# Kernel tuning notes

Measured on AMD Instinct MI355X. Metric: run time of the kernel, lower is better.

The kernel has to match this reference:

```python
import jax, jax.numpy as jnp
import numpy as np

D_MODEL = 1024
NUM_HEADS = 16
HEAD_DIM = D_MODEL // NUM_HEADS
R = 1.0
LAM = 0.1
CLIP_MIN = -15.0
CLIP_MAX = 15.0
EPS = 1e-9


def setup_inputs() -> dict:
    key = jax.random.key(0)
    k1, k2 = jax.random.split(key, 2)
    B, S = 2, 2048
    x = jax.random.normal(k1, (B, S, D_MODEL), dtype=jnp.float32)
    # NonNeg-constrained dense kernel -> nonnegative uniform init (small scale)
    W = jax.random.uniform(k2, (D_MODEL, D_MODEL), dtype=jnp.float32) * 0.02
    b = jnp.zeros((D_MODEL,), dtype=jnp.float32)
    d_q = jnp.ones((D_MODEL,), dtype=jnp.float32)
    d_k = jnp.ones((D_MODEL,), dtype=jnp.float32)
    d_v = jnp.ones((D_MODEL,), dtype=jnp.float32)
    return {"x": x, "W": W, "b": b, "d_q": d_q, "d_k": d_k, "d_v": d_v}


def _convex_r_softmax(z):
    z = jnp.clip(z, CLIP_MIN, CLIP_MAX)
    numerator = jax.nn.relu(jnp.exp(z - R) + LAM * z)
    denominator = jnp.sum(numerator, axis=-1, keepdims=True) + EPS
    return numerator / denominator


def reference(x, W, b, d_q, d_k, d_v):
    B, S, _ = x.shape
    x_proj = x @ W + b                      # [B, S, D]
    # diagonal scaling then split heads: [B, H, S, Dh]
    def heads(t):
        return t.reshape(B, S, NUM_HEADS, HEAD_DIM).transpose(0, 2, 1, 3)
    Q = heads(x_proj * d_q)
    K = heads(x_proj * d_k)
    V = heads(x_proj * d_v)
    scores = jnp.einsum('bhqd,bhkd->bhqk', Q, K)   # [B, H, S, S]
    attn = _convex_r_softmax(scores)
    out = jnp.einsum('bhqk,bhkd->bhqd', attn, V)   # [B, H, S, Dh]
    return out.transpose(0, 2, 1, 3).reshape(B, S, D_MODEL)
```

## Files before the change

kernel.cpp:

```cpp
#include <hip/hip_runtime.h>
#include <math.h>

#define D_MODEL   1024
#define NUM_HEADS 16
#define HEAD_DIM  64
#define S_LEN     2048
#define BATCH     2
#define M_TOT     (BATCH * S_LEN)

typedef __attribute__((ext_vector_type(8))) short short8;
typedef __attribute__((ext_vector_type(4))) short short4v;
typedef __attribute__((ext_vector_type(4))) float f32x4;

static __device__ __forceinline__ short f2bf(float f) {
    unsigned u = __builtin_bit_cast(unsigned, f);
    unsigned r = (u + 0x7FFFu + ((u >> 16) & 1u)) >> 16;
    return (short)r;
}

typedef __attribute__((address_space(3))) void lds_v;
typedef const __attribute__((address_space(1))) void glb_v;
static __device__ __forceinline__ void gll16(const void* g, void* l) {
    __builtin_amdgcn_global_load_lds((glb_v*)g, (lds_v*)l, 16, 0, 0);
}


__global__ __launch_bounds__(256) void cvt_x_kernel(
    const float* __restrict__ x, short* __restrict__ xb)
{
    int i = (blockIdx.x * 256 + threadIdx.x) * 8;
    float4 a = *(const float4*)(x + i);
    float4 b = *(const float4*)(x + i + 4);
    short8 o;
    o[0] = f2bf(a.x); o[1] = f2bf(a.y); o[2] = f2bf(a.z); o[3] = f2bf(a.w);
    o[4] = f2bf(b.x); o[5] = f2bf(b.y); o[6] = f2bf(b.z); o[7] = f2bf(b.w);
    *(short8*)(xb + i) = o;
}

__global__ __launch_bounds__(256) void cvt_w_kernel(
    const float* __restrict__ W, short* __restrict__ wt)
{
    __shared__ short T[64][72];
    const int tid = threadIdx.x;
    const int k0 = blockIdx.y * 64, n0 = blockIdx.x * 64;
    const int r = tid >> 4, c4 = (tid & 15) * 4;
    #pragma unroll
    for (int i = 0; i < 4; i++) {
        int kr = r + 16 * i;
        float4 v = *(const float4*)(W + (size_t)(k0 + kr) * D_MODEL + n0 + c4);
        short4v s;
        s[0] = f2bf(v.x); s[1] = f2bf(v.y); s[2] = f2bf(v.z); s[3] = f2bf(v.w);
        *(short4v*)&T[kr][c4] = s;
    }
    __syncthreads();
    const int n = tid >> 2, kb = (tid & 3) * 16;
    short tmp[16];
    #pragma unroll
    for (int j = 0; j < 16; j++) tmp[j] = T[kb + j][n];
    *(short8*)(wt + (size_t)(n0 + n) * D_MODEL + k0 + kb)     = *(short8*)&tmp[0];
    *(short8*)(wt + (size_t)(n0 + n) * D_MODEL + k0 + kb + 8) = *(short8*)&tmp[8];
}

__global__ __launch_bounds__(256) void gemm_qkv_kernel(
    const short* __restrict__ xb, const short* __restrict__ wt,
    const float* __restrict__ bias, const float* __restrict__ dq,
    const float* __restrict__ dk, const float* __restrict__ dv,
    short* __restrict__ Q, short* __restrict__ K, short* __restrict__ Vt)
{
    __shared__ __attribute__((aligned(16))) short lds[17408];

    const int tid  = threadIdx.x;
    const int w    = tid >> 6, l = tid & 63;
    const int quad = l >> 4,  c = l & 15;
    const int cx   = c & 7;
    const int n0 = blockIdx.x * 128, m0 = blockIdx.y * 128;
    const int wm = (w & 1) * 64, wn = (w >> 1) * 64;
    short* As = lds;
    short* Bs = lds + 8192;

    const int srow  = l >> 3;
    const int sslot = (l & 7) ^ srow;

    f32x4 acc[4][4];
    #pragma unroll
    for (int mi = 0; mi < 4; mi++)
        #pragma unroll
        for (int ni = 0; ni < 4; ni++) acc[mi][ni] = (f32x4){0.f, 0.f, 0.f, 0.f};

    for (int k0 = 0; k0 < D_MODEL; k0 += 64) {
        __syncthreads();
        #pragma unroll
        for (int i = 0; i < 4; i++) {
            int rbase = w * 32 + i * 8;
            int row = rbase + srow;
            gll16(xb + (size_t)(m0 + row) * D_MODEL + k0 + sslot * 8, As + rbase * 64);
            gll16(wt + (size_t)(n0 + row) * D_MODEL + k0 + sslot * 8, Bs + rbase * 64);
        }
        __syncthreads();
        #pragma unroll
        for (int kh = 0; kh < 2; kh++) {
            const int sx = (kh * 4 + quad) ^ cx;
            short8 af[4], bf[4];
            #pragma unroll
            for (int mi = 0; mi < 4; mi++)
                af[mi] = *(const short8*)&As[(wm + 16 * mi + c) * 64 + sx * 8];
            #pragma unroll
            for (int ni = 0; ni < 4; ni++)
                bf[ni] = *(const short8*)&Bs[(wn + 16 * ni + c) * 64 + sx * 8];
            #pragma unroll
            for (int mi = 0; mi < 4; mi++)
                #pragma unroll
                for (int ni = 0; ni < 4; ni++)
                    acc[mi][ni] = __builtin_amdgcn_mfma_f32_16x16x32_bf16(
                        af[mi], bf[ni], acc[mi][ni], 0, 0, 0);
        }
    }

    __syncthreads();
    const int b      = m0 >> 11;
    const int s_base = m0 & 2047;
    const int h      = (n0 + wn) >> 6;

    float biasv[4], dqv[4], dkv[4], dvv[4];
    #pragma unroll
    for (int ni = 0; ni < 4; ni++) {
        int n_g = n0 + wn + 16 * ni + c;
        biasv[ni] = bias[n_g]; dqv[ni] = dq[n_g];
        dkv[ni] = dk[n_g];     dvv[ni] = dv[n_g];
    }

    short* E = lds;
    #pragma unroll
    for (int mi = 0; mi < 4; mi++) {
        #pragma unroll
        for (int ni = 0; ni < 4; ni++) {
            short4v vv;
            #pragma unroll
            for (int r = 0; r < 4; r++) {
                float xv = acc[mi][ni][r] + biasv[ni];
                int s = s_base + wm + 16 * mi + 4 * quad + r;
                size_t off = (((size_t)(b * NUM_HEADS + h) * S_LEN + s) << 6) + (16 * ni + c);
                Q[off] = f2bf(xv * dqv[ni]);
                K[off] = f2bf(xv * dkv[ni]);
                vv[r]  = f2bf(xv * dvv[ni]);
            }
            int n_l = wn + 16 * ni + c;
            int m_l = wm + 16 * mi + 4 * quad;
            *(short4v*)&E[n_l * 136 + m_l] = vv;
        }
    }
    __syncthreads();
    {
        const int n_l = tid >> 1, mh = (tid & 1) * 64;
        const int h2 = (n0 + n_l) >> 6;
        const int dh = n_l & 63;
        short* dst = Vt + ((size_t)(b * NUM_HEADS + h2) * HEAD_DIM + dh) * S_LEN + s_base;
        #pragma unroll
        for (int ch = 0; ch < 8; ch++) {
            short8 v = *(const short8*)&E[n_l * 136 + mh + ch * 8];
            *(short8*)(dst + mh + ch * 8) = v;
        }
    }
}

__global__ __launch_bounds__(256) void attn2_kernel(
    const short* __restrict__ Q, const short* __restrict__ K,
    const short* __restrict__ Vt, float* __restrict__ out)
{
    __shared__ __attribute__((aligned(16))) short lds[8192 + 4 * 16 * 88];

    const int tid  = threadIdx.x;
    const int w    = tid >> 6, l = tid & 63;
    const int quad = l >> 4,  c = l & 15;
    const int cx   = c & 7;
    const int q0 = blockIdx.x * 64;
    const int h  = blockIdx.y, b = blockIdx.z;
    const size_t bh = (size_t)(b * NUM_HEADS + h);
    const short* Qh  = Q  + bh * S_LEN * HEAD_DIM;
    const short* Kh  = K  + bh * S_LEN * HEAD_DIM;
    const short* Vth = Vt + bh * HEAD_DIM * S_LEN;

    short* Ks = lds;
    short* Vs = lds + 4096;
    short* Ps = lds + 8192 + w * (16 * 88);

    const int srow  = l >> 3;
    const int sslot = (l & 7) ^ srow;

    short8 qf[2];
    {
        const short* qp = Qh + (size_t)(q0 + 16 * w + c) * 64 + quad * 8;
        qf[0] = *(const short8*)(qp);
        qf[1] = *(const short8*)(qp + 32);
    }

    f32x4 acc_o[4];
    #pragma unroll
    for (int i = 0; i < 4; i++) acc_o[i] = (f32x4){0.f, 0.f, 0.f, 0.f};
    float dnm = 0.0f;

    for (int kt = 0; kt < S_LEN / 64; kt++) {
        const int k0 = kt * 64;
        __syncthreads();
        #pragma unroll
        for (int i = 0; i < 2; i++) {
            int rbase = 16 * w + 8 * i;
            int row = rbase + srow;
            gll16(Kh + (size_t)(k0 + row) * 64 + sslot * 8, Ks + rbase * 64);
            gll16(Vth + (size_t)row * S_LEN + k0 + sslot * 8, Vs + rbase * 64);
        }
        __syncthreads();

        f32x4 sacc[4];
        #pragma unroll
        for (int n = 0; n < 4; n++) sacc[n] = (f32x4){0.f, 0.f, 0.f, 0.f};
        #pragma unroll
        for (int hh = 0; hh < 2; hh++) {
            const int sx = (hh * 4 + quad) ^ cx;
            #pragma unroll
            for (int n = 0; n < 4; n++) {
                short8 kf = *(const short8*)&Ks[(16 * n + c) * 64 + sx * 8];
                sacc[n] = __builtin_amdgcn_mfma_f32_16x16x32_bf16(kf, qf[hh], sacc[n], 0, 0, 0);
            }
        }

        #pragma unroll
        for (int n = 0; n < 4; n++) {
            float nm[4];
            #pragma unroll
            for (int r = 0; r < 4; r++) {
                float z = __builtin_amdgcn_fmed3f(sacc[n][r], -15.0f, 15.0f);
                float e = __builtin_amdgcn_exp2f(
                    __builtin_fmaf(z, 1.4426950408889634f, -1.4426950408889634f));
                float num = fmaxf(__builtin_fmaf(z, 0.1f, e), 0.0f);
                dnm += num;
                nm[r] = num;
            }
            unsigned p0 = __builtin_amdgcn_perm(
                __builtin_bit_cast(unsigned, nm[1]) + 0x8000u,
                __builtin_bit_cast(unsigned, nm[0]) + 0x8000u, 0x07060302u);
            unsigned p1 = __builtin_amdgcn_perm(
                __builtin_bit_cast(unsigned, nm[3]) + 0x8000u,
                __builtin_bit_cast(unsigned, nm[2]) + 0x8000u, 0x07060302u);
            uint2 pr; pr.x = p0; pr.y = p1;
            *(uint2*)&Ps[c * 88 + 16 * n + 4 * quad] = pr;
        }

        #pragma unroll
        for (int kh = 0; kh < 2; kh++) {
            short8 pf = *(const short8*)&Ps[c * 88 + 32 * kh + 8 * quad];
            const int sx = (kh * 4 + quad) ^ cx;
            #pragma unroll
            for (int n2 = 0; n2 < 4; n2++) {
                short8 vf = *(const short8*)&Vs[(16 * n2 + c) * 64 + sx * 8];
                acc_o[n2] = __builtin_amdgcn_mfma_f32_16x16x32_bf16(pf, vf, acc_o[n2], 0, 0, 0);
            }
        }
    }

    dnm += __shfl_xor(dnm, 16, 64);
    dnm += __shfl_xor(dnm, 32, 64);

    #pragma unroll
    for (int r = 0; r < 4; r++) {
        float dr  = __shfl(dnm, quad * 4 + r, 64);
        float inv = 1.0f / (dr + 1e-9f);
        int qrow = q0 + 16 * w + 4 * quad + r;
        float* op = out + ((size_t)(b * S_LEN + qrow) << 10) + (h << 6) + c;
        #pragma unroll
        for (int n2 = 0; n2 < 4; n2++)
            op[16 * n2] = acc_o[n2][r] * inv;
    }
}

__global__ __launch_bounds__(256, 4) void gemm_xw_kernel(
    const float* __restrict__ x, const float* __restrict__ W,
    const float* __restrict__ bias, float* __restrict__ xp)
{
    __shared__ float Asf[64][36];
    __shared__ float Bsf[32][68];

    const int tid = threadIdx.x;
    const int tx  = tid & 15;
    const int ty  = tid >> 4;
    const int m0  = blockIdx.y * 64;
    const int n0  = blockIdx.x * 64;

    float acc[4][4];
    #pragma unroll
    for (int i = 0; i < 4; i++)
        #pragma unroll
        for (int j = 0; j < 4; j++) acc[i][j] = 0.0f;

    for (int k0 = 0; k0 < D_MODEL; k0 += 32) {
        #pragma unroll
        for (int i = 0; i < 2; i++) {
            int idx = tid + i * 256;
            int r = idx >> 3, c4 = idx & 7;
            *(float4*)(&Asf[r][c4 * 4]) =
                *(const float4*)(x + (size_t)(m0 + r) * D_MODEL + k0 + c4 * 4);
        }
        #pragma unroll
        for (int i = 0; i < 2; i++) {
            int idx = tid + i * 256;
            int r = idx >> 4, c4 = idx & 15;
            *(float4*)(&Bsf[r][c4 * 4]) =
                *(const float4*)(W + (size_t)(k0 + r) * D_MODEL + n0 + c4 * 4);
        }
        __syncthreads();
        #pragma unroll
        for (int k = 0; k < 32; k += 4) {
            float a[4][4];
            #pragma unroll
            for (int i = 0; i < 4; i++) {
                float4 t = *(const float4*)(&Asf[ty + 16 * i][k]);
                a[i][0] = t.x; a[i][1] = t.y; a[i][2] = t.z; a[i][3] = t.w;
            }
            #pragma unroll
            for (int kk = 0; kk < 4; kk++) {
                float4 bv = *(const float4*)(&Bsf[k + kk][tx * 4]);
                #pragma unroll
                for (int i = 0; i < 4; i++) {
                    acc[i][0] += a[i][kk] * bv.x;
                    acc[i][1] += a[i][kk] * bv.y;
                    acc[i][2] += a[i][kk] * bv.z;
                    acc[i][3] += a[i][kk] * bv.w;
                }
            }
        }
        __syncthreads();
    }
    float4 bv = *(const float4*)(bias + n0 + tx * 4);
    #pragma unroll
    for (int i = 0; i < 4; i++) {
        float4 r;
        r.x = acc[i][0] + bv.x; r.y = acc[i][1] + bv.y;
        r.z = acc[i][2] + bv.z; r.w = acc[i][3] + bv.w;
        *(float4*)(xp + (size_t)(m0 + ty + 16 * i) * D_MODEL + n0 + tx * 4) = r;
    }
}

__global__ __launch_bounds__(256, 4) void attn_fb_kernel(
    const float* __restrict__ xp, const float* __restrict__ dq,
    const float* __restrict__ dk, const float* __restrict__ dv,
    float* __restrict__ out)
{
    __shared__ __attribute__((aligned(16))) short lds[13824];

    const int tid  = threadIdx.x;
    const int wave = tid >> 6;
    const int l    = tid & 63;
    const int quad = l >> 4;
    const int c    = l & 15;
    const int q0   = blockIdx.x * 64;
    const int h    = blockIdx.y;
    const int bb   = blockIdx.z;
    const int col0 = h * HEAD_DIM;
    const float* base = xp + (size_t)bb * S_LEN * D_MODEL;

    short* Ks = lds;
    short* Vt = lds + 64 * 72;
    short* Ps = lds + 2 * 64 * 72 + wave * (16 * 72);

    short8 qf[2];
    {
        const int qrow = q0 + wave * 16 + c;
        const float* qp = base + (size_t)qrow * D_MODEL + col0 + quad * 8;
        const float* sp = dq + col0 + quad * 8;
        #pragma unroll
        for (int hh = 0; hh < 2; hh++) {
            float4 v0 = *(const float4*)(qp + 32 * hh);
            float4 v1 = *(const float4*)(qp + 32 * hh + 4);
            float4 s0 = *(const float4*)(sp + 32 * hh);
            float4 s1 = *(const float4*)(sp + 32 * hh + 4);
            qf[hh][0] = f2bf(v0.x * s0.x); qf[hh][1] = f2bf(v0.y * s0.y);
            qf[hh][2] = f2bf(v0.z * s0.z); qf[hh][3] = f2bf(v0.w * s0.w);
            qf[hh][4] = f2bf(v1.x * s1.x); qf[hh][5] = f2bf(v1.y * s1.y);
            qf[hh][6] = f2bf(v1.z * s1.z); qf[hh][7] = f2bf(v1.w * s1.w);
        }
    }

    const int sc4  = 4 * (tid & 15);
    const int srow = tid >> 4;
    const float4 ksc = *(const float4*)(dk + col0 + sc4);
    const int vd = tid & 63;
    const int vg = tid >> 6;
    const float vsc = dv[col0 + vd];

    f32x4 acc_o[4];
    #pragma unroll
    for (int i = 0; i < 4; i++) acc_o[i] = (f32x4){0.f, 0.f, 0.f, 0.f};
    float dnm = 0.0f;

    for (int kt = 0; kt < S_LEN / 64; kt++) {
        const int k0 = kt * 64;
        __syncthreads();

        #pragma unroll
        for (int i = 0; i < 4; i++) {
            int r = srow + 16 * i;
            float4 v = *(const float4*)(base + (size_t)(k0 + r) * D_MODEL + col0 + sc4);
            short4v s;
            s[0] = f2bf(v.x * ksc.x); s[1] = f2bf(v.y * ksc.y);
            s[2] = f2bf(v.z * ksc.z); s[3] = f2bf(v.w * ksc.w);
            *(short4v*)&Ks[r * 72 + sc4] = s;
        }
        #pragma unroll
        for (int p = 0; p < 4; p++) {
            int kb = 16 * p + 4 * vg;
            const float* vp = base + (size_t)(k0 + kb) * D_MODEL + col0 + vd;
            float a0 = vp[0 * D_MODEL], a1 = vp[1 * D_MODEL];
            float a2 = vp[2 * D_MODEL], a3 = vp[3 * D_MODEL];
            short4v s;
            s[0] = f2bf(a0 * vsc); s[1] = f2bf(a1 * vsc);
            s[2] = f2bf(a2 * vsc); s[3] = f2bf(a3 * vsc);
            *(short4v*)&Vt[vd * 72 + kb] = s;
        }
        __syncthreads();

        f32x4 sacc[4];
        #pragma unroll
        for (int n = 0; n < 4; n++) sacc[n] = (f32x4){0.f, 0.f, 0.f, 0.f};
        #pragma unroll
        for (int n = 0; n < 4; n++)
            #pragma unroll
            for (int hh = 0; hh < 2; hh++) {
                short8 kf = *(const short8*)&Ks[(16 * n + c) * 72 + 32 * hh + 8 * quad];
                sacc[n] = __builtin_amdgcn_mfma_f32_16x16x32_bf16(kf, qf[hh], sacc[n], 0, 0, 0);
            }

        #pragma unroll
        for (int n = 0; n < 4; n++) {
            short4v pp;
            #pragma unroll
            for (int r = 0; r < 4; r++) {
                float z = fminf(fmaxf(sacc[n][r], -15.0f), 15.0f);
                float e = __expf(z - 1.0f);
                float num = fmaxf(fmaf(z, 0.1f, e), 0.0f);
                dnm += num;
                pp[r] = f2bf(num);
            }
            *(short4v*)&Ps[c * 72 + 16 * n + 4 * quad] = pp;
        }

        #pragma unroll
        for (int kh = 0; kh < 2; kh++) {
            short8 pf = *(const short8*)&Ps[c * 72 + 32 * kh + 8 * quad];
            #pragma unroll
            for (int n2 = 0; n2 < 4; n2++) {
                short8 vf = *(const short8*)&Vt[(16 * n2 + c) * 72 + 32 * kh + 8 * quad];
                acc_o[n2] = __builtin_amdgcn_mfma_f32_16x16x32_bf16(pf, vf, acc_o[n2], 0, 0, 0);
            }
        }
    }

    dnm += __shfl_xor(dnm, 16, 64);
    dnm += __shfl_xor(dnm, 32, 64);

    #pragma unroll
    for (int r = 0; r < 4; r++) {
        float dr  = __shfl(dnm, quad * 4 + r, 64);
        float inv = 1.0f / (dr + 1e-9f);
        const int qrow = q0 + wave * 16 + quad * 4 + r;
        float* op = out + (size_t)(bb * S_LEN + qrow) * D_MODEL + col0 + c;
        #pragma unroll
        for (int n2 = 0; n2 < 4; n2++)
            op[16 * n2] = acc_o[n2][r] * inv;
    }
}

extern "C" void kernel_launch(void* const* d_in, const int* in_sizes, int n_in,
                              void* d_out, int out_size, void* d_ws, size_t ws_size,
                              hipStream_t stream) {
    const float* x  = (const float*)d_in[0];
    const float* W  = (const float*)d_in[1];
    const float* bias = (const float*)d_in[2];
    const float* dq = (const float*)d_in[3];
    const float* dk = (const float*)d_in[4];
    const float* dv = (const float*)d_in[5];
    float* out = (float*)d_out;

    const size_t XB_B = (size_t)M_TOT * D_MODEL * 2;
    const size_t WT_B = (size_t)D_MODEL * D_MODEL * 2;
    const size_t T_B  = (size_t)BATCH * NUM_HEADS * S_LEN * HEAD_DIM * 2;
    const size_t NEED = XB_B + WT_B + 3 * T_B;

    if (ws_size >= NEED) {
        char* p = (char*)d_ws;
        short* xb = (short*)p;             p += XB_B;
        short* wt = (short*)p;             p += WT_B;
        short* Qt = (short*)p;             p += T_B;
        short* Kt = (short*)p;             p += T_B;
        short* Vt = (short*)p;

        cvt_x_kernel<<<(M_TOT * D_MODEL) / 2048, 256, 0, stream>>>(x, xb);
        dim3 gw(D_MODEL / 64, D_MODEL / 64);
        cvt_w_kernel<<<gw, 256, 0, stream>>>(W, wt);
        dim3 gg(D_MODEL / 128, M_TOT / 128);
        gemm_qkv_kernel<<<gg, 256, 0, stream>>>(xb, wt, bias, dq, dk, dv, Qt, Kt, Vt);
        dim3 ga(S_LEN / 64, NUM_HEADS, BATCH);
        attn2_kernel<<<ga, 256, 0, stream>>>(Qt, Kt, Vt, out);
    } else {
        float* xp = (float*)d_ws;
        dim3 g1(D_MODEL / 64, M_TOT / 64);
        gemm_xw_kernel<<<g1, 256, 0, stream>>>(x, W, bias, xp);
        dim3 g2(S_LEN / 64, NUM_HEADS, BATCH);
        attn_fb_kernel<<<g2, 256, 0, stream>>>(xp, dq, dk, dv, out);
    }
}
```

Measured before the change: 173.4 us.

## Double query rows per attention warp and halve GEMM M-tile

The attention kernel now gives each warp 32 query rows (two 16-row sub-tiles) instead of 16. Each K/V tile loaded into LDS is reused across twice as many queries, halving the number of blocks and the total K/V global traffic, and each K/V fragment read feeds two MFMAs. Separately, the QKV projection GEMM tile shrinks from 128x128 to 64x128, doubling the block count to improve occupancy and load balance. The cost is higher register pressure and LDS use in attention, and fewer attention blocks (512), which may underfill the GPU's compute units.

```diff
diff --git a/kernel.cpp b/kernel.cpp
--- a/kernel.cpp
+++ b/kernel.cpp
@@ -67,48 +67,53 @@
     const float* __restrict__ dk, const float* __restrict__ dv,
     short* __restrict__ Q, short* __restrict__ K, short* __restrict__ Vt)
 {
-    __shared__ __attribute__((aligned(16))) short lds[17408];
+    __shared__ __attribute__((aligned(16))) short lds[12288];
 
     const int tid  = threadIdx.x;
     const int w    = tid >> 6, l = tid & 63;
     const int quad = l >> 4,  c = l & 15;
     const int cx   = c & 7;
-    const int n0 = blockIdx.x * 128, m0 = blockIdx.y * 128;
-    const int wm = (w & 1) * 64, wn = (w >> 1) * 64;
+    const int n0 = blockIdx.x * 128, m0 = blockIdx.y * 64;
+    const int wm = (w & 1) * 32, wn = (w >> 1) * 64;
     short* As = lds;
-    short* Bs = lds + 8192;
+    short* Bs = lds + 4096;
 
     const int srow  = l >> 3;
     const int sslot = (l & 7) ^ srow;
 
-    f32x4 acc[4][4];
-    #pragma unroll
-    for (int mi = 0; mi < 4; mi++)
+    f32x4 acc[2][4];
+    #pragma unroll
+    for (int mi = 0; mi < 2; mi++)
         #pragma unroll
         for (int ni = 0; ni < 4; ni++) acc[mi][ni] = (f32x4){0.f, 0.f, 0.f, 0.f};
 
     for (int k0 = 0; k0 < D_MODEL; k0 += 64) {
         __syncthreads();
         #pragma unroll
+        for (int i = 0; i < 2; i++) {
+            int rbase = 16 * w + 8 * i;
+            gll16(xb + (size_t)(m0 + rbase + srow) * D_MODEL + k0 + sslot * 8,
+                  As + rbase * 64);
+        }
+        #pragma unroll
         for (int i = 0; i < 4; i++) {
-            int rbase = w * 32 + i * 8;
-            int row = rbase + srow;
-            gll16(xb + (size_t)(m0 + row) * D_MODEL + k0 + sslot * 8, As + rbase * 64);
-            gll16(wt + (size_t)(n0 + row) * D_MODEL + k0 + sslot * 8, Bs + rbase * 64);
+            int rbase = 32 * w + 8 * i;
+            gll16(wt + (size_t)(n0 + rbase + srow) * D_MODEL + k0 + sslot * 8,
+                  Bs + rbase * 64);
         }
         __syncthreads();
         #pragma unroll
         for (int kh = 0; kh < 2; kh++) {
             const int sx = (kh * 4 + quad) ^ cx;
-            short8 af[4], bf[4];
-            #pragma unroll
-            for (int mi = 0; mi < 4; mi++)
+            short8 af[2], bf[4];
+            #pragma unroll
+            for (int mi = 0; mi < 2; mi++)
                 af[mi] = *(const short8*)&As[(wm + 16 * mi + c) * 64 + sx * 8];
             #pragma unroll
             for (int ni = 0; ni < 4; ni++)
                 bf[ni] = *(const short8*)&Bs[(wn + 16 * ni + c) * 64 + sx * 8];
             #pragma unroll
-            for (int mi = 0; mi < 4; mi++)
+            for (int mi = 0; mi < 2; mi++)
                 #pragma unroll
                 for (int ni = 0; ni < 4; ni++)
                     acc[mi][ni] = __builtin_amdgcn_mfma_f32_16x16x32_bf16(
@@ -131,7 +136,7 @@
 
     short* E = lds;
     #pragma unroll
-    for (int mi = 0; mi < 4; mi++) {
+    for (int mi = 0; mi < 2; mi++) {
         #pragma unroll
         for (int ni = 0; ni < 4; ni++) {
             short4v vv;
@@ -146,18 +151,18 @@
             }
             int n_l = wn + 16 * ni + c;
             int m_l = wm + 16 * mi + 4 * quad;
-            *(short4v*)&E[n_l * 136 + m_l] = vv;
+            *(short4v*)&E[n_l * 72 + m_l] = vv;
         }
     }
     __syncthreads();
     {
-        const int n_l = tid >> 1, mh = (tid & 1) * 64;
+        const int n_l = tid >> 1, mh = (tid & 1) * 32;
         const int h2 = (n0 + n_l) >> 6;
         const int dh = n_l & 63;
         short* dst = Vt + ((size_t)(b * NUM_HEADS + h2) * HEAD_DIM + dh) * S_LEN + s_base;
         #pragma unroll
-        for (int ch = 0; ch < 8; ch++) {
-            short8 v = *(const short8*)&E[n_l * 136 + mh + ch * 8];
+        for (int ch = 0; ch < 4; ch++) {
+            short8 v = *(const short8*)&E[n_l * 72 + mh + ch * 8];
             *(short8*)(dst + mh + ch * 8) = v;
         }
     }
@@ -167,13 +172,13 @@
     const short* __restrict__ Q, const short* __restrict__ K,
     const short* __restrict__ Vt, float* __restrict__ out)
 {
-    __shared__ __attribute__((aligned(16))) short lds[8192 + 4 * 16 * 88];
+    __shared__ __attribute__((aligned(16))) short lds[8192 + 4 * 32 * 88];
 
     const int tid  = threadIdx.x;
     const int w    = tid >> 6, l = tid & 63;
     const int quad = l >> 4,  c = l & 15;
     const int cx   = c & 7;
-    const int q0 = blockIdx.x * 64;
+    const int q0 = blockIdx.x * 128;
     const int h  = blockIdx.y, b = blockIdx.z;
     const size_t bh = (size_t)(b * NUM_HEADS + h);
     const short* Qh  = Q  + bh * S_LEN * HEAD_DIM;
@@ -182,22 +187,28 @@
 
     short* Ks = lds;
     short* Vs = lds + 4096;
-    short* Ps = lds + 8192 + w * (16 * 88);
+    short* Ps = lds + 8192 + w * (32 * 88);
 
     const int srow  = l >> 3;
     const int sslot = (l & 7) ^ srow;
 
-    short8 qf[2];
+    short8 qf0[2], qf1[2];
     {
-        const short* qp = Qh + (size_t)(q0 + 16 * w + c) * 64 + quad * 8;
-        qf[0] = *(const short8*)(qp);
-        qf[1] = *(const short8*)(qp + 32);
-    }
-
-    f32x4 acc_o[4];
-    #pragma unroll
-    for (int i = 0; i < 4; i++) acc_o[i] = (f32x4){0.f, 0.f, 0.f, 0.f};
-    float dnm = 0.0f;
+        const short* qp0 = Qh + (size_t)(q0 + 32 * w + c) * 64 + quad * 8;
+        const short* qp1 = qp0 + 16 * 64;
+        qf0[0] = *(const short8*)(qp0);
+        qf0[1] = *(const short8*)(qp0 + 32);
+        qf1[0] = *(const short8*)(qp1);
+        qf1[1] = *(const short8*)(qp1 + 32);
+    }
+
+    f32x4 o0[4], o1[4];
+    #pragma unroll
+    for (int i = 0; i < 4; i++) {
+        o0[i] = (f32x4){0.f, 0.f, 0.f, 0.f};
+        o1[i] = (f32x4){0.f, 0.f, 0.f, 0.f};
+    }
+    float dnm0 = 0.0f, dnm1 = 0.0f;
 
     for (int kt = 0; kt < S_LEN / 64; kt++) {
         const int k0 = kt * 64;
@@ -211,16 +222,20 @@
         }
         __syncthreads();
 
-        f32x4 sacc[4];
-        #pragma unroll
-        for (int n = 0; n < 4; n++) sacc[n] = (f32x4){0.f, 0.f, 0.f, 0.f};
+        f32x4 s0[4], s1[4];
+        #pragma unroll
+        for (int n = 0; n < 4; n++) {
+            s0[n] = (f32x4){0.f, 0.f, 0.f, 0.f};
+            s1[n] = (f32x4){0.f, 0.f, 0.f, 0.f};
+        }
         #pragma unroll
         for (int hh = 0; hh < 2; hh++) {
             const int sx = (hh * 4 + quad) ^ cx;
             #pragma unroll
             for (int n = 0; n < 4; n++) {
                 short8 kf = *(const short8*)&Ks[(16 * n + c) * 64 + sx * 8];
-                sacc[n] = __builtin_amdgcn_mfma_f32_16x16x32_bf16(kf, qf[hh], sacc[n], 0, 0, 0);
+                s0[n] = __builtin_amdgcn_mfma_f32_16x16x32_bf16(kf, qf0[hh], s0[n], 0, 0, 0);
+                s1[n] = __builtin_amdgcn_mfma_f32_16x16x32_bf16(kf, qf1[hh], s1[n], 0, 0, 0);
             }
         }
 
@@ -229,11 +244,11 @@
             float nm[4];
             #pragma unroll
             for (int r = 0; r < 4; r++) {
-                float z = __builtin_amdgcn_fmed3f(sacc[n][r], -15.0f, 15.0f);
+                float z = __builtin_amdgcn_fmed3f(s0[n][r], -15.0f, 15.0f);
                 float e = __builtin_amdgcn_exp2f(
                     __builtin_fmaf(z, 1.4426950408889634f, -1.4426950408889634f));
                 float num = fmaxf(__builtin_fmaf(z, 0.1f, e), 0.0f);
-                dnm += num;
+                dnm0 += num;
                 nm[r] = num;
             }
             unsigned p0 = __builtin_amdgcn_perm(
@@ -245,31 +260,61 @@
             uint2 pr; pr.x = p0; pr.y = p1;
             *(uint2*)&Ps[c * 88 + 16 * n + 4 * quad] = pr;
         }
+        #pragma unroll
+        for (int n = 0; n < 4; n++) {
+            float nm[4];
+            #pragma unroll
+            for (int r = 0; r < 4; r++) {
+                float z = __builtin_amdgcn_fmed3f(s1[n][r], -15.0f, 15.0f);
+                float e = __builtin_amdgcn_exp2f(
+                    __builtin_fmaf(z, 1.4426950408889634f, -1.4426950408889634f));
+                float num = fmaxf(__builtin_fmaf(z, 0.1f, e), 0.0f);
+                dnm1 += num;
+                nm[r] = num;
+            }
+            unsigned p0 = __builtin_amdgcn_perm(
+                __builtin_bit_cast(unsigned, nm[1]) + 0x8000u,
+                __builtin_bit_cast(unsigned, nm[0]) + 0x8000u, 0x07060302u);
+            unsigned p1 = __builtin_amdgcn_perm(
+                __builtin_bit_cast(unsigned, nm[3]) + 0x8000u,
+                __builtin_bit_cast(unsigned, nm[2]) + 0x8000u, 0x07060302u);
+            uint2 pr; pr.x = p0; pr.y = p1;
+            *(uint2*)&Ps[(16 + c) * 88 + 16 * n + 4 * quad] = pr;
+        }
 
         #pragma unroll
         for (int kh = 0; kh < 2; kh++) {
-            short8 pf = *(const short8*)&Ps[c * 88 + 32 * kh + 8 * quad];
+            short8 pf0 = *(const short8*)&Ps[c * 88 + 32 * kh + 8 * quad];
+            short8 pf1 = *(const short8*)&Ps[(16 + c) * 88 + 32 * kh + 8 * quad];
             const int sx = (kh * 4 + quad) ^ cx;
             #pragma unroll
             for (int n2 = 0; n2 < 4; n2++) {
                 short8 vf = *(const short8*)&Vs[(16 * n2 + c) * 64 + sx * 8];
-                acc_o[n2] = __builtin_amdgcn_mfma_f32_16x16x32_bf16(pf, vf, acc_o[n2], 0, 0, 0);
-            }
-        }
-    }
-
-    dnm += __shfl_xor(dnm, 16, 64);
-    dnm += __shfl_xor(dnm, 32, 64);
+                o0[n2] = __builtin_amdgcn_mfma_f32_16x16x32_bf16(pf0, vf, o0[n2], 0, 0, 0);
+                o1[n2] = __builtin_amdgcn_mfma_f32_16x16x32_bf16(pf1, vf, o1[n2], 0, 0, 0);
+            }
+        }
+    }
+
+    dnm0 += __shfl_xor(dnm0, 16, 64);
+    dnm0 += __shfl_xor(dnm0, 32, 64);
+    dnm1 += __shfl_xor(dnm1, 16, 64);
+    dnm1 += __shfl_xor(dnm1, 32, 64);
 
     #pragma unroll
     for (int r = 0; r < 4; r++) {
-        float dr  = __shfl(dnm, quad * 4 + r, 64);
-        float inv = 1.0f / (dr + 1e-9f);
-        int qrow = q0 + 16 * w + 4 * quad + r;
-        float* op = out + ((size_t)(b * S_LEN + qrow) << 10) + (h << 6) + c;
-        #pragma unroll
-        for (int n2 = 0; n2 < 4; n2++)
-            op[16 * n2] = acc_o[n2][r] * inv;
+        float dr0 = __shfl(dnm0, quad * 4 + r, 64);
+        float dr1 = __shfl(dnm1, quad * 4 + r, 64);
+        float inv0 = 1.0f / (dr0 + 1e-9f);
+        float inv1 = 1.0f / (dr1 + 1e-9f);
+        int qrow0 = q0 + 32 * w + 4 * quad + r;
+        float* op0 = out + ((size_t)(b * S_LEN + qrow0) << 10) + (h << 6) + c;
+        float* op1 = op0 + (16 << 10);
+        #pragma unroll
+        for (int n2 = 0; n2 < 4; n2++) {
+            op0[16 * n2] = o0[n2][r] * inv0;
+            op1[16 * n2] = o1[n2][r] * inv1;
+        }
     }
 }
 
@@ -496,9 +541,9 @@
         cvt_x_kernel<<<(M_TOT * D_MODEL) / 2048, 256, 0, stream>>>(x, xb);
         dim3 gw(D_MODEL / 64, D_MODEL / 64);
         cvt_w_kernel<<<gw, 256, 0, stream>>>(W, wt);
-        dim3 gg(D_MODEL / 128, M_TOT / 128);
+        dim3 gg(D_MODEL / 128, M_TOT / 64);
         gemm_qkv_kernel<<<gg, 256, 0, stream>>>(xb, wt, bias, dq, dk, dv, Qt, Kt, Vt);
-        dim3 ga(S_LEN / 64, NUM_HEADS, BATCH);
+        dim3 ga(S_LEN / 128, NUM_HEADS, BATCH);
         attn2_kernel<<<ga, 256, 0, stream>>>(Qt, Kt, Vt, out);
     } else {
         float* xp = (float*)d_ws;
```

Result: faster. 167.4 us (-3.4%).
